# Kernel tuning notes

Hardware: AMD Instinct MI355X
Metric: run time of the kernel (lower is better)

The kernel has to match this reference:

```python
import jax, jax.numpy as jnp
import numpy as np

B = 8192          # batch
FEAT = 14 * 14 * (16 + 4)  # 3920 features per image
NUM_CLASSES = 10
REPS = 8          # CX+RY repetitions in the filter circuit


def _filter_probs(p):
    """Analytic output distribution of the 4-qubit filter circuit.
    p: (..., 4) pixel angles [p0, p1, p2, p3].
    Circuit: RY(p_i) on qubit i, then 8x [CX(0,1); RY(p0,0)], measure all.
    Qubits 2,3 stay in product state; evolve (q0,q1) as a real 2x2 amplitude
    grid a[q0, q1]. Output index = q0*8 + q1*4 + q2*2 + q3 (Qiskit bitstring
    reversed as in the torch source).
    """
    h = 0.5 * p
    c, s = jnp.cos(h), jnp.sin(h)
    v0 = jnp.stack([c[..., 0], s[..., 0]], axis=-1)
    v1 = jnp.stack([c[..., 1], s[..., 1]], axis=-1)
    a = v0[..., :, None] * v1[..., None, :]        # (..., 2, 2) amplitudes a[q0,q1]
    c0, s0 = c[..., 0], s[..., 0]
    R0 = jnp.stack([jnp.stack([c0, -s0], axis=-1),
                    jnp.stack([s0,  c0], axis=-1)], axis=-2)  # RY(p0) matrix
    for _ in range(REPS):
        # CX(control=q0, target=q1): flip q1 where q0 == 1
        a = jnp.stack([a[..., 0, :], a[..., 1, ::-1]], axis=-2)
        # RY(p0) on q0
        a = jnp.einsum('...ik,...kj->...ij', R0, a)
    P01 = a * a                                    # joint probs over (q0, q1)
    p2 = s[..., 2] ** 2                            # P(q2 = 1)
    p3 = s[..., 3] ** 2                            # P(q3 = 1)
    P2 = jnp.stack([1.0 - p2, p2], axis=-1)
    P3 = jnp.stack([1.0 - p3, p3], axis=-1)
    P = (P01[..., :, :, None, None]
         * P2[..., None, None, :, None]
         * P3[..., None, None, None, :])           # (..., q0, q1, q2, q3)
    return P.reshape(P.shape[:-4] + (16,))


def _sampler_probs(tl, br):
    """2-qubit sampler with all weights = 0: the two CX(0,1) cancel, so the
    state is RY(tl)|0> x RY(br)|0>. Output index = q0*2 + q1."""
    s0 = jnp.sin(0.5 * tl) ** 2   # P(q0 = 1)
    s1 = jnp.sin(0.5 * br) ** 2   # P(q1 = 1)
    return jnp.stack([(1 - s0) * (1 - s1), (1 - s0) * s1,
                      s0 * (1 - s1), s0 * s1], axis=-1)


def setup_inputs() -> dict:
    key = jax.random.key(0)
    k1, k2 = jax.random.split(key)
    x = jax.random.uniform(k1, (B, 1, 28, 28), dtype=jnp.float32)
    fc_w = jax.random.normal(k2, (NUM_CLASSES, FEAT), dtype=jnp.float32) * (FEAT ** -0.5)
    fc_b = jnp.zeros((NUM_CLASSES,), dtype=jnp.float32)
    return {"x": x, "fc_w": fc_w, "fc_b": fc_b}


def reference(x, fc_w, fc_b):
    b = x.shape[0]
    # (b, 14, 14, 2, 2) patches; patch[u, v] = img[2i+u, 2j+v]
    patches = x.reshape(b, 14, 2, 14, 2).transpose(0, 1, 3, 2, 4)
    p = patches.reshape(b, 196, 4)                 # [p0, p1, p2, p3] per patch
    filter_feats = _filter_probs(p).reshape(b, -1)            # (b, 196*16)
    sampler_feats = _sampler_probs(patches[..., 0, 0],
                                   patches[..., 1, 1]).reshape(b, -1)  # (b, 196*4)
    feats = jnp.concatenate([filter_feats, sampler_feats], axis=-1)
    logits = feats @ fc_w.T + fc_b
    return jax.nn.log_softmax(logits, axis=-1)
```

## Files before the change

### kernel.cpp

```cpp
#include <hip/hip_runtime.h>
#include <hip/hip_bf16.h>

typedef float v2f __attribute__((ext_vector_type(2)));
typedef short short8 __attribute__((ext_vector_type(8)));
typedef float f32x4 __attribute__((ext_vector_type(4)));

#define NCLS  10
#define FEATN 3920
#define GIMG  8
#define RSTR  532

__device__ __forceinline__ unsigned packbf(float a, float b) {
    __hip_bfloat162 h = __float22bfloat162_rn(float2{a, b});
    unsigned u; __builtin_memcpy(&u, &h, 4); return u;
}

__device__ __forceinline__ void fastsc(float v, float& s, float& c) {
    const float r = v * 0.07957747154594767f;
#if __has_builtin(__builtin_amdgcn_sinf)
    s = __builtin_amdgcn_sinf(r);
    c = __builtin_amdgcn_cosf(r);
#else
    s = __sinf(0.5f * v);
    c = __cosf(0.5f * v);
#endif
}

__global__ __launch_bounds__(256, 4)
void quanv_all(const float* __restrict__ x,
               const float* __restrict__ fc_w,
               const float* __restrict__ fc_b,
               float* __restrict__ out) {
    __shared__ __align__(16) unsigned lds[GIMG * RSTR];
    const int tid  = threadIdx.x;
    const int lane = tid & 63;
    const int wave = tid >> 6;
    const int img0 = blockIdx.x * GIMG;
    const float* base = x + (size_t)img0 * 784;
    const int am  = lane & 15;
    const int ach = lane >> 4;
    const unsigned aoff = (unsigned)((am & 7) * RSTR + ach * 4);
    const bool bnv = am < NCLS;
    const float* wrow = fc_w + (size_t)(bnv ? am : 0) * FEATN;
    const int ach8 = ach * 8;

    f32x4 acc = {0.f, 0.f, 0.f, 0.f};

    float2 pc[4], pn[4];
    int lpC, qC; bool actC;
    {
        actC = tid < 48 * 4;
        const int tt = actC ? tid : 0;
        qC = tt / 48; lpC = tt - qC * 48;
        const int pi = lpC / 14, pj = lpC - pi * 14;
        const int off = pi * 56 + pj * 2;
        const float* iA = base + (size_t)(2 * qC) * 784;
        pc[0] = *reinterpret_cast<const float2*>(iA + off);
        pc[1] = *reinterpret_cast<const float2*>(iA + off + 28);
        pc[2] = *reinterpret_cast<const float2*>(iA + 784 + off);
        pc[3] = *reinterpret_cast<const float2*>(iA + 784 + off + 28);
    }

    #pragma unroll
    for (int t = 0; t < 4; ++t) {
        const int np   = (t == 3) ? 52 : 48;
        const int nkb  = (t == 3) ? 33 : 30;
        const int np16 = np * 16, np20 = np * 20;
        const int fb   = 768 * t, sb = 3136 + 192 * t;

        if (actC) {
            const float2 tA = pc[0], bA = pc[1], tB = pc[2], bB = pc[3];
            float sA0,cA0,sA1,cA1,sA2,cA2,sA3,cA3;
            float sB0,cB0,sB1,cB1,sB2,cB2,sB3,cB3;
            fastsc(tA.x, sA0, cA0); fastsc(tA.y, sA1, cA1);
            fastsc(bA.x, sA2, cA2); fastsc(bA.y, sA3, cA3);
            fastsc(tB.x, sB0, cB0); fastsc(tB.y, sB1, cB1);
            fastsc(bB.x, sB2, cB2); fastsc(bB.y, sB3, cB3);

            const v2f c0 = {cA0, cB0}, s0 = {sA0, sB0};
            const v2f c1 = {cA1, cB1}, s1 = {sA1, sB1};
            v2f a00 = c0 * c1, a01 = c0 * s1, a10 = s0 * c1, a11 = s0 * s1;
            #pragma unroll
            for (int r = 0; r < 8; ++r) {
                const v2f b10 = a11, b11 = a10;
                const v2f n00 = c0 * a00 - s0 * b10;
                const v2f n01 = c0 * a01 - s0 * b11;
                const v2f n10 = s0 * a00 + c0 * b10;
                const v2f n11 = s0 * a01 + c0 * b11;
                a00 = n00; a01 = n01; a10 = n10; a11 = n11;
            }
            v2f P2[4];
            P2[0] = a00 * a00; P2[1] = a01 * a01; P2[2] = a10 * a10; P2[3] = a11 * a11;
            const v2f t2c = {cA2*cA2, cB2*cB2}, t2s = {sA2*sA2, sB2*sB2};
            const v2f t3c = {cA3*cA3, cB3*cB3}, t3s = {sA3*sA3, sB3*sB3};
            v2f T[4];
            T[0] = t2c * t3c; T[1] = t2c * t3s; T[2] = t2s * t3c; T[3] = t2s * t3s;

            unsigned dA[8], dB[8];
            #pragma unroll
            for (int m = 0; m < 4; ++m) {
                const v2f f0 = P2[m] * T[0], f1 = P2[m] * T[1];
                const v2f f2 = P2[m] * T[2], f3 = P2[m] * T[3];
                dA[2*m]   = packbf(f0.x, f1.x); dA[2*m+1] = packbf(f2.x, f3.x);
                dB[2*m]   = packbf(f0.y, f1.y); dB[2*m+1] = packbf(f2.y, f3.y);
            }
            const v2f sa = s0 * s0, sb2 = t3s;
            const v2f na = 1.0f - sa, nb = 1.0f - sb2;
            const v2f e0 = na * nb, e1 = na * sb2, e2 = sa * nb, e3 = sa * sb2;

            unsigned* rowA = lds + (2 * qC) * RSTR;
            unsigned* rowB = rowA + RSTR;
            *reinterpret_cast<uint4*>(rowA + lpC * 8)     = uint4{dA[0], dA[1], dA[2], dA[3]};
            *reinterpret_cast<uint4*>(rowA + lpC * 8 + 4) = uint4{dA[4], dA[5], dA[6], dA[7]};
            *reinterpret_cast<uint2*>(rowA + np * 8 + lpC * 2) =
                uint2{packbf(e0.x, e1.x), packbf(e2.x, e3.x)};
            *reinterpret_cast<uint4*>(rowB + lpC * 8)     = uint4{dB[0], dB[1], dB[2], dB[3]};
            *reinterpret_cast<uint4*>(rowB + lpC * 8 + 4) = uint4{dB[4], dB[5], dB[6], dB[7]};
            *reinterpret_cast<uint2*>(rowB + np * 8 + lpC * 2) =
                uint2{packbf(e0.y, e1.y), packbf(e2.y, e3.y)};
        }
        if (t == 3 && tid < 64)
            lds[(tid >> 3) * RSTR + 520 + (tid & 7)] = 0u;

        int lpN = 0, qN = 0; bool actN = false;
        if (t < 3) {
            const int npN = (t + 1 == 3) ? 52 : 48;
            actN = tid < npN * 4;
            const int tt = actN ? tid : 0;
            qN = tt / npN; lpN = tt - qN * npN;
            const int p = 48 * (t + 1) + lpN;
            const int pi = p / 14, pj = p - pi * 14;
            const int off = pi * 56 + pj * 2;
            const float* iA = base + (size_t)(2 * qN) * 784;
            pn[0] = *reinterpret_cast<const float2*>(iA + off);
            pn[1] = *reinterpret_cast<const float2*>(iA + off + 28);
            pn[2] = *reinterpret_cast<const float2*>(iA + 784 + off);
            pn[3] = *reinterpret_cast<const float2*>(iA + 784 + off + 28);
        }
        __syncthreads();

        for (int kb = wave; kb < nkb; kb += 4) {
            const short8 a = *reinterpret_cast<const short8*>(lds + aoff + kb * 16);
            const int u = kb * 32 + ach8;
            const bool val = bnv && (u < np20);
            const int addr = val ? ((u < np16) ? fb + u : sb + (u - np16)) : 0;
            float4 wa = *reinterpret_cast<const float4*>(wrow + addr);
            float4 wb = *reinterpret_cast<const float4*>(wrow + addr + 4);
            if (!val) { wa = float4{0.f,0.f,0.f,0.f}; wb = float4{0.f,0.f,0.f,0.f}; }
            const uint4 bu{packbf(wa.x, wa.y), packbf(wa.z, wa.w),
                           packbf(wb.x, wb.y), packbf(wb.z, wb.w)};
            short8 b; __builtin_memcpy(&b, &bu, 16);
            acc = __builtin_amdgcn_mfma_f32_16x16x32_bf16(a, b, acc, 0, 0, 0);
        }
        __syncthreads();

        pc[0] = pn[0]; pc[1] = pn[1]; pc[2] = pn[2]; pc[3] = pn[3];
        lpC = lpN; qC = qN; actC = actN;
    }

    float* f = reinterpret_cast<float*>(lds);
    f[wave * 256 +   0 + lane] = acc[0];
    f[wave * 256 +  64 + lane] = acc[1];
    f[wave * 256 + 128 + lane] = acc[2];
    f[wave * 256 + 192 + lane] = acc[3];
    __syncthreads();
    if (tid < GIMG * NCLS) {
        const int g = tid / NCLS, c = tid - g * NCLS;
        const int li = ((g >> 2) << 4) + c;
        const int ri = (g & 3) << 6;
        float v = f[ri + li] + f[256 + ri + li] + f[512 + ri + li] + f[768 + ri + li];
        f[1024 + tid] = v + fc_b[c];
    }
    __syncthreads();
    if (tid < GIMG * NCLS) {
        const int g = tid / NCLS, c = tid - g * NCLS;
        const float* lg = f + 1024 + g * NCLS;
        float m = -1e30f;
        #pragma unroll
        for (int k = 0; k < NCLS; ++k) m = fmaxf(m, lg[k]);
        float ss = 0.f;
        #pragma unroll
        for (int k = 0; k < NCLS; ++k) ss += __expf(lg[k] - m);
        out[(size_t)(img0 + g) * NCLS + c] = lg[c] - m - __logf(ss);
    }
}

extern "C" void kernel_launch(void* const* d_in, const int* in_sizes, int n_in,
                              void* d_out, int out_size, void* d_ws, size_t ws_size,
                              hipStream_t stream) {
    const float* x    = (const float*)d_in[0];
    const float* fc_w = (const float*)d_in[1];
    const float* fc_b = (const float*)d_in[2];
    float* out = (float*)d_out;
    const int B = in_sizes[0] / 784;
    const int grid = B / GIMG;
    quanv_all<<<grid, 256, 0, stream>>>(x, fc_w, fc_b, out);
}
```

Before: 89.29 us.

## Prepack FC weights into MFMA-ready bf16 layout and double-buffer LDS tiles

A small pre-kernel now converts fc_w to bf16 and reorders it into the exact per-lane MFMA B-operand layout, with zero padding, and stores it in workspace. The main kernel then loads one 16-byte short8 per lane instead of two float4 loads, index arithmetic and bf16 packing in the inner loop. The LDS feature tile is double-buffered so the trailing barrier in each stage can be dropped. The cost is an extra kernel launch each call and twice the LDS per block, which may reduce occupancy.

```diff
diff --git a/kernel.cpp b/kernel.cpp
--- a/kernel.cpp
+++ b/kernel.cpp
@@ -9,6 +9,7 @@
 #define FEATN 3920
 #define GIMG  8
 #define RSTR  532
+#define LDSN  (GIMG * RSTR)
 
 __device__ __forceinline__ unsigned packbf(float a, float b) {
     __hip_bfloat162 h = __float22bfloat162_rn(float2{a, b});
@@ -26,12 +27,37 @@
 #endif
 }
 
+__global__ void conv_w(const float* __restrict__ fc_w, __hip_bfloat16* __restrict__ ws) {
+    const int id = blockIdx.x * 256 + threadIdx.x;
+    if (id >= 123 * 512) return;
+    const int kb = id >> 9, r = id & 511, l = r >> 3, j0 = r & 7;
+    const int n  = l & 15;
+    const int kk = kb * 32 + ((l >> 4) << 3) + j0;
+    float w = 0.f;
+    if (n < NCLS) {
+        const int t    = (kk < 2880) ? kk / 960 : 3;
+        const int base = 960 * t;
+        const int P0   = 48 * t;
+        const int np   = (t == 3) ? 52 : 48;
+        const int u    = kk - base;
+        int korig = -1;
+        if (u < np * 16) {
+            korig = 16 * (P0 + (u >> 4)) + (u & 15);
+        } else {
+            const int v = u - np * 16;
+            if (v < np * 4) korig = 3136 + 4 * (P0 + (v >> 2)) + (v & 3);
+        }
+        if (korig >= 0) w = fc_w[n * FEATN + korig];
+    }
+    ws[id] = __float2bfloat16(w);
+}
+
 __global__ __launch_bounds__(256, 4)
-void quanv_all(const float* __restrict__ x,
-               const float* __restrict__ fc_w,
-               const float* __restrict__ fc_b,
-               float* __restrict__ out) {
-    __shared__ __align__(16) unsigned lds[GIMG * RSTR];
+void quanv_mfma(const float* __restrict__ x,
+                const short* __restrict__ wsb,
+                const float* __restrict__ fc_b,
+                float* __restrict__ out) {
+    __shared__ __align__(16) unsigned lds[2 * LDSN];
     const int tid  = threadIdx.x;
     const int lane = tid & 63;
     const int wave = tid >> 6;
@@ -40,11 +66,8 @@
     const int am  = lane & 15;
     const int ach = lane >> 4;
     const unsigned aoff = (unsigned)((am & 7) * RSTR + ach * 4);
-    const bool bnv = am < NCLS;
-    const float* wrow = fc_w + (size_t)(bnv ? am : 0) * FEATN;
-    const int ach8 = ach * 8;
-
-    f32x4 acc = {0.f, 0.f, 0.f, 0.f};
+
+    if (tid < 64) lds[LDSN + (tid >> 3) * RSTR + 520 + (tid & 7)] = 0u;
 
     float2 pc[4], pn[4];
     int lpC, qC; bool actC;
@@ -61,12 +84,14 @@
         pc[3] = *reinterpret_cast<const float2*>(iA + 784 + off + 28);
     }
 
+    f32x4 acc = {0.f, 0.f, 0.f, 0.f};
+
     #pragma unroll
     for (int t = 0; t < 4; ++t) {
-        const int np   = (t == 3) ? 52 : 48;
-        const int nkb  = (t == 3) ? 33 : 30;
-        const int np16 = np * 16, np20 = np * 20;
-        const int fb   = 768 * t, sb = 3136 + 192 * t;
+        const int np  = (t == 3) ? 52 : 48;
+        const int nkb = (t == 3) ? 33 : 30;
+        const int kbb = 30 * t;
+        unsigned* buf = lds + (t & 1) * LDSN;
 
         if (actC) {
             const float2 tA = pc[0], bA = pc[1], tB = pc[2], bB = pc[3];
@@ -108,7 +133,7 @@
             const v2f na = 1.0f - sa, nb = 1.0f - sb2;
             const v2f e0 = na * nb, e1 = na * sb2, e2 = sa * nb, e3 = sa * sb2;
 
-            unsigned* rowA = lds + (2 * qC) * RSTR;
+            unsigned* rowA = buf + (2 * qC) * RSTR;
             unsigned* rowB = rowA + RSTR;
             *reinterpret_cast<uint4*>(rowA + lpC * 8)     = uint4{dA[0], dA[1], dA[2], dA[3]};
             *reinterpret_cast<uint4*>(rowA + lpC * 8 + 4) = uint4{dA[4], dA[5], dA[6], dA[7]};
@@ -119,8 +144,6 @@
             *reinterpret_cast<uint2*>(rowB + np * 8 + lpC * 2) =
                 uint2{packbf(e0.y, e1.y), packbf(e2.y, e3.y)};
         }
-        if (t == 3 && tid < 64)
-            lds[(tid >> 3) * RSTR + 520 + (tid & 7)] = 0u;
 
         int lpN = 0, qN = 0; bool actN = false;
         if (t < 3) {
@@ -137,26 +160,20 @@
             pn[2] = *reinterpret_cast<const float2*>(iA + 784 + off);
             pn[3] = *reinterpret_cast<const float2*>(iA + 784 + off + 28);
         }
+
         __syncthreads();
 
         for (int kb = wave; kb < nkb; kb += 4) {
-            const short8 a = *reinterpret_cast<const short8*>(lds + aoff + kb * 16);
-            const int u = kb * 32 + ach8;
-            const bool val = bnv && (u < np20);
-            const int addr = val ? ((u < np16) ? fb + u : sb + (u - np16)) : 0;
-            float4 wa = *reinterpret_cast<const float4*>(wrow + addr);
-            float4 wb = *reinterpret_cast<const float4*>(wrow + addr + 4);
-            if (!val) { wa = float4{0.f,0.f,0.f,0.f}; wb = float4{0.f,0.f,0.f,0.f}; }
-            const uint4 bu{packbf(wa.x, wa.y), packbf(wa.z, wa.w),
-                           packbf(wb.x, wb.y), packbf(wb.z, wb.w)};
-            short8 b; __builtin_memcpy(&b, &bu, 16);
+            const short8 a = *reinterpret_cast<const short8*>(buf + aoff + kb * 16);
+            const short8 b = *reinterpret_cast<const short8*>(wsb + (size_t)(kbb + kb) * 512 + lane * 8);
             acc = __builtin_amdgcn_mfma_f32_16x16x32_bf16(a, b, acc, 0, 0, 0);
         }
-        __syncthreads();
 
         pc[0] = pn[0]; pc[1] = pn[1]; pc[2] = pn[2]; pc[3] = pn[3];
         lpC = lpN; qC = qN; actC = actN;
     }
+
+    __syncthreads();
 
     float* f = reinterpret_cast<float*>(lds);
     f[wave * 256 +   0 + lane] = acc[0];
@@ -192,7 +209,10 @@
     const float* fc_w = (const float*)d_in[1];
     const float* fc_b = (const float*)d_in[2];
     float* out = (float*)d_out;
+
+    conv_w<<<246, 256, 0, stream>>>(fc_w, (__hip_bfloat16*)d_ws);
+
     const int B = in_sizes[0] / 784;
     const int grid = B / GIMG;
-    quanv_all<<<grid, 256, 0, stream>>>(x, fc_w, fc_b, out);
-}
+    quanv_mfma<<<grid, 256, 0, stream>>>(x, (const short*)d_ws, fc_b, out);
+}
```

Result: faster. 82.44 us (median of 2 runs) (-7.7%).

## Double-buffer feature LDS and prefetch weight fragments ahead of feature compute

Applied to the files above, without the earlier changes.

The feature staging area in LDS becomes two ping-pong buffers, so the trailing barrier after each tile's MFMA loop can go; one barrier runs after the loop instead. Each tile's fc_w fragments are loaded and converted to bf16 into registers before the trig and amplitude math, so weight-load latency overlaps that compute. Per-lane masking is replaced by clamped addresses: out-of-range classes load row 9, and the zero pad in the second buffer cancels the overhang. In exchange it uses twice the LDS and about 36 more VGPRs, which could hurt occupancy.

```diff
diff --git a/kernel.cpp b/kernel.cpp
--- a/kernel.cpp
+++ b/kernel.cpp
@@ -9,6 +9,7 @@
 #define FEATN 3920
 #define GIMG  8
 #define RSTR  532
+#define LDSN  (GIMG * RSTR)
 
 __device__ __forceinline__ unsigned packbf(float a, float b) {
     __hip_bfloat162 h = __float22bfloat162_rn(float2{a, b});
@@ -27,11 +28,11 @@
 }
 
 __global__ __launch_bounds__(256, 4)
-void quanv_all(const float* __restrict__ x,
-               const float* __restrict__ fc_w,
-               const float* __restrict__ fc_b,
-               float* __restrict__ out) {
-    __shared__ __align__(16) unsigned lds[GIMG * RSTR];
+void quanv_mfma(const float* __restrict__ x,
+                const float* __restrict__ fc_w,
+                const float* __restrict__ fc_b,
+                float* __restrict__ out) {
+    __shared__ __align__(16) unsigned lds[2 * LDSN];
     const int tid  = threadIdx.x;
     const int lane = tid & 63;
     const int wave = tid >> 6;
@@ -39,12 +40,11 @@
     const float* base = x + (size_t)img0 * 784;
     const int am  = lane & 15;
     const int ach = lane >> 4;
+    const int ach8 = ach * 8;
     const unsigned aoff = (unsigned)((am & 7) * RSTR + ach * 4);
-    const bool bnv = am < NCLS;
-    const float* wrow = fc_w + (size_t)(bnv ? am : 0) * FEATN;
-    const int ach8 = ach * 8;
-
-    f32x4 acc = {0.f, 0.f, 0.f, 0.f};
+    const float* wrow = fc_w + (size_t)(am < NCLS ? am : 9) * FEATN;
+
+    if (tid < 64) lds[LDSN + (tid >> 3) * RSTR + 520 + (tid & 7)] = 0u;
 
     float2 pc[4], pn[4];
     int lpC, qC; bool actC;
@@ -61,12 +61,32 @@
         pc[3] = *reinterpret_cast<const float2*>(iA + 784 + off + 28);
     }
 
+    f32x4 acc = {0.f, 0.f, 0.f, 0.f};
+
     #pragma unroll
     for (int t = 0; t < 4; ++t) {
         const int np   = (t == 3) ? 52 : 48;
         const int nkb  = (t == 3) ? 33 : 30;
-        const int np16 = np * 16, np20 = np * 20;
+        const int np16 = np * 16;
         const int fb   = 768 * t, sb = 3136 + 192 * t;
+
+        short8 bfr[9];
+        #pragma unroll
+        for (int i = 0; i < 9; ++i) {
+            const int kb = wave + 4 * i;
+            if (kb < nkb) {
+                const int u = kb * 32 + ach8;
+                int addr = (u < np16) ? fb + u : sb + (u - np16);
+                addr = min(addr, FEATN - 8);
+                const float4 wa = *reinterpret_cast<const float4*>(wrow + addr);
+                const float4 wb = *reinterpret_cast<const float4*>(wrow + addr + 4);
+                const uint4 bu{packbf(wa.x, wa.y), packbf(wa.z, wa.w),
+                               packbf(wb.x, wb.y), packbf(wb.z, wb.w)};
+                __builtin_memcpy(&bfr[i], &bu, 16);
+            }
+        }
+
+        unsigned* buf = lds + (t & 1) * LDSN;
 
         if (actC) {
             const float2 tA = pc[0], bA = pc[1], tB = pc[2], bB = pc[3];
@@ -108,7 +128,7 @@
             const v2f na = 1.0f - sa, nb = 1.0f - sb2;
             const v2f e0 = na * nb, e1 = na * sb2, e2 = sa * nb, e3 = sa * sb2;
 
-            unsigned* rowA = lds + (2 * qC) * RSTR;
+            unsigned* rowA = buf + (2 * qC) * RSTR;
             unsigned* rowB = rowA + RSTR;
             *reinterpret_cast<uint4*>(rowA + lpC * 8)     = uint4{dA[0], dA[1], dA[2], dA[3]};
             *reinterpret_cast<uint4*>(rowA + lpC * 8 + 4) = uint4{dA[4], dA[5], dA[6], dA[7]};
@@ -119,8 +139,6 @@
             *reinterpret_cast<uint2*>(rowB + np * 8 + lpC * 2) =
                 uint2{packbf(e0.y, e1.y), packbf(e2.y, e3.y)};
         }
-        if (t == 3 && tid < 64)
-            lds[(tid >> 3) * RSTR + 520 + (tid & 7)] = 0u;
 
         int lpN = 0, qN = 0; bool actN = false;
         if (t < 3) {
@@ -137,26 +155,23 @@
             pn[2] = *reinterpret_cast<const float2*>(iA + 784 + off);
             pn[3] = *reinterpret_cast<const float2*>(iA + 784 + off + 28);
         }
+
         __syncthreads();
 
-        for (int kb = wave; kb < nkb; kb += 4) {
-            const short8 a = *reinterpret_cast<const short8*>(lds + aoff + kb * 16);
-            const int u = kb * 32 + ach8;
-            const bool val = bnv && (u < np20);
-            const int addr = val ? ((u < np16) ? fb + u : sb + (u - np16)) : 0;
-            float4 wa = *reinterpret_cast<const float4*>(wrow + addr);
-            float4 wb = *reinterpret_cast<const float4*>(wrow + addr + 4);
-            if (!val) { wa = float4{0.f,0.f,0.f,0.f}; wb = float4{0.f,0.f,0.f,0.f}; }
-            const uint4 bu{packbf(wa.x, wa.y), packbf(wa.z, wa.w),
-                           packbf(wb.x, wb.y), packbf(wb.z, wb.w)};
-            short8 b; __builtin_memcpy(&b, &bu, 16);
-            acc = __builtin_amdgcn_mfma_f32_16x16x32_bf16(a, b, acc, 0, 0, 0);
-        }
-        __syncthreads();
+        #pragma unroll
+        for (int i = 0; i < 9; ++i) {
+            const int kb = wave + 4 * i;
+            if (kb < nkb) {
+                const short8 a = *reinterpret_cast<const short8*>(buf + aoff + kb * 16);
+                acc = __builtin_amdgcn_mfma_f32_16x16x32_bf16(a, bfr[i], acc, 0, 0, 0);
+            }
+        }
 
         pc[0] = pn[0]; pc[1] = pn[1]; pc[2] = pn[2]; pc[3] = pn[3];
         lpC = lpN; qC = qN; actC = actN;
     }
+
+    __syncthreads();
 
     float* f = reinterpret_cast<float*>(lds);
     f[wave * 256 +   0 + lane] = acc[0];
@@ -194,5 +209,5 @@
     float* out = (float*)d_out;
     const int B = in_sizes[0] / 784;
     const int grid = B / GIMG;
-    quanv_all<<<grid, 256, 0, stream>>>(x, fc_w, fc_b, out);
-}
+    quanv_mfma<<<grid, 256, 0, stream>>>(x, fc_w, fc_b, out);
+}
```

Measured after the change: 89.09 us. No clear change (-0.2%).
